# Performance work log

Measured on AMD Instinct MI355X. Metric: run time of the kernel, lower is better.

The kernel has to match this reference:

```python
import jax, jax.numpy as jnp
import numpy as np

NUM_HEADS = 32  # head_dim = input_dim // num_heads = 32 == C (forced by matmul contraction)


def setup_inputs() -> dict:
    key = jax.random.key(0)
    ks = jax.random.split(key, 8)
    B, C, D3, H1 = 16, 32, 1, 32
    input_dim = 1024  # == C**2, forced by the final view(B, C, H1, W1)
    s = 0.02
    x1 = jax.random.normal(ks[0], (B, C, D3, H1, input_dim), jnp.float32)
    x2 = jax.random.normal(ks[1], (B, C, D3, H1, input_dim), jnp.float32)
    Wq = jax.random.normal(ks[2], (input_dim, input_dim), jnp.float32) * s
    bq = jax.random.normal(ks[3], (input_dim,), jnp.float32) * s
    Wk = jax.random.normal(ks[4], (input_dim, input_dim), jnp.float32) * s
    bk = jax.random.normal(ks[5], (input_dim,), jnp.float32) * s
    Wv = jax.random.normal(ks[6], (input_dim, input_dim), jnp.float32) * s
    bv = jax.random.normal(ks[7], (input_dim,), jnp.float32) * s
    return {"x1": x1, "x2": x2, "Wq": Wq, "bq": bq, "Wk": Wk, "bk": bk, "Wv": Wv, "bv": bv}


def reference(x1, x2, Wq, bq, Wk, bk, Wv, bv):
    B, C, _, H1, W1 = x1.shape  # W1 == input_dim (Linear acts on last dim)
    nh = NUM_HEADS
    hd = W1 // nh
    # Linear projections on the last axis (torch Linear: x @ W.T + b)
    q = (x1 @ Wq.T + bq).reshape(B, C, nh, hd, -1).transpose(0, 2, 4, 3, 1)  # (B, nh, L1, hd, C)
    k = (x2 @ Wk.T + bk).reshape(B, C, nh, hd, -1)                            # (B, C, nh, hd, L2)
    v = (x2 @ Wv.T + bv).reshape(B, C, nh, hd, -1)                            # (B, C, nh, hd, L2)
    # Broadcasted batched matmul: contracts q's trailing C axis with k's hd axis (C == hd).
    energy = jnp.matmul(q, k)                      # (B, C, L1, hd, L2)
    attention = jax.nn.softmax(energy, axis=-1)    # softmax over L2
    # Contracts v's L2 axis with attention's hd axis (L2 == hd).
    out = jnp.matmul(v, attention)                 # (B, C, L1, hd, L2)
    out = out.transpose(0, 2, 4, 3, 1).reshape(B, C, H1, W1)
    return out
```

## Files before the change

### kernel.cpp

```cpp
#include <hip/hip_runtime.h>
#include <cstdint>

typedef __bf16 bf16x8 __attribute__((ext_vector_type(8)));
typedef float f32x4 __attribute__((ext_vector_type(4)));
typedef unsigned short us8 __attribute__((ext_vector_type(8)));

__device__ __forceinline__ unsigned short f2bf(float f) {
  union { float f; uint32_t u; } c; c.f = f;
  uint32_t u = c.u + 0x7FFFu + ((c.u >> 16) & 1u);
  return (unsigned short)(u >> 16);
}

__global__ __launch_bounds__(256) void cvt5(
    const float* __restrict__ x1, const float* __restrict__ x2,
    const float* __restrict__ Wq, const float* __restrict__ Wk, const float* __restrict__ Wv,
    unsigned short* __restrict__ xb1, unsigned short* __restrict__ xb2,
    unsigned short* __restrict__ wb) {
  int z = blockIdx.y;
  const float* src; unsigned short* dst; int n4;
  if (z == 0)      { src = x1; dst = xb1;            n4 = 16777216 / 4; }
  else if (z == 1) { src = x2; dst = xb2;            n4 = 16777216 / 4; }
  else if (z == 2) { src = Wq; dst = wb;             n4 = 1048576 / 4; }
  else if (z == 3) { src = Wk; dst = wb + 1048576;   n4 = 1048576 / 4; }
  else             { src = Wv; dst = wb + 2*1048576; n4 = 1048576 / 4; }
  for (int i = blockIdx.x * 256 + threadIdx.x; i < n4; i += gridDim.x * 256) {
    float4 v = ((const float4*)src)[i];
    ushort4 o;
    o.x = f2bf(v.x); o.y = f2bf(v.y); o.z = f2bf(v.z); o.w = f2bf(v.w);
    ((ushort4*)dst)[i] = o;
  }
}

__global__ __launch_bounds__(256) void gemm_qkv(
    const unsigned short* __restrict__ xb1, const unsigned short* __restrict__ xb2,
    const unsigned short* __restrict__ wb,
    const float* __restrict__ bq, const float* __restrict__ bk, const float* __restrict__ bv,
    unsigned short* __restrict__ qkv) {
  __shared__ __attribute__((aligned(16))) unsigned short lA[128 * 32];
  __shared__ __attribute__((aligned(16))) unsigned short lB[128 * 32];
  const int id = blockIdx.x;
  const int xcd = id & 7;
  const int j = id >> 3;
  const int nb = j & 7;
  const int g = j >> 3;
  const int z = g >> 4;
  const int mb = (g & 15) * 8 + xcd;
  const unsigned short* A = (z == 0) ? xb1 : xb2;
  const unsigned short* W = wb + z * 1048576;
  const float* bias = (z == 0) ? bq : (z == 1 ? bk : bv);
  unsigned short* C = qkv + z * 16777216;
  const int n0 = nb * 128;
  const int m0 = mb * 128;
  const int lane = threadIdx.x & 63;
  const int wv = threadIdx.x >> 6;
  const int wm = wv >> 1, wn = wv & 1;
  const int mr = lane & 15, quad = lane >> 4;

  f32x4 acc[4][4];
#pragma unroll
  for (int i = 0; i < 4; ++i)
#pragma unroll
    for (int jj = 0; jj < 4; ++jj) acc[i][jj] = (f32x4){0.f, 0.f, 0.f, 0.f};

  for (int k0 = 0; k0 < 1024; k0 += 32) {
#pragma unroll
    for (int c4 = 0; c4 < 4; ++c4) {
      int c = wv * 4 + c4;
      int isB = c >> 3;
      int cc = c & 7;
      int row = cc * 16 + (lane >> 2);
      const unsigned short* src = isB ? (W + (n0 + row) * 1024 + k0)
                                      : (A + (m0 + row) * 1024 + k0);
      const char* gp = (const char*)src + (lane & 3) * 16;
      char* ldst = (char*)(isB ? lB : lA) + cc * 1024;
      __builtin_amdgcn_global_load_lds((const __attribute__((address_space(1))) void*)gp,
                                       (__attribute__((address_space(3))) void*)ldst,
                                       16, 0, 0);
    }
    __syncthreads();
    bf16x8 af[4], bfr[4];
#pragma unroll
    for (int i = 0; i < 4; ++i)
      af[i] = *(const bf16x8*)(lA + (wm * 64 + i * 16 + mr) * 32 + quad * 8);
#pragma unroll
    for (int jj = 0; jj < 4; ++jj)
      bfr[jj] = *(const bf16x8*)(lB + (wn * 64 + jj * 16 + mr) * 32 + quad * 8);
#pragma unroll
    for (int i = 0; i < 4; ++i)
#pragma unroll
      for (int jj = 0; jj < 4; ++jj)
        acc[i][jj] = __builtin_amdgcn_mfma_f32_16x16x32_bf16(af[i], bfr[jj], acc[i][jj], 0, 0, 0);
    __syncthreads();
  }
#pragma unroll
  for (int jj = 0; jj < 4; ++jj) {
    int col = n0 + wn * 64 + jj * 16 + mr;
    float bb = bias[col];
#pragma unroll
    for (int i = 0; i < 4; ++i) {
      int rbase = m0 + wm * 64 + i * 16 + quad * 4;
#pragma unroll
      for (int r = 0; r < 4; ++r)
        C[(rbase + r) * 1024 + col] = f2bf(acc[i][jj][r] + bb);
    }
  }
}

__global__ __launch_bounds__(256) void attn(const unsigned short* __restrict__ qkv,
                                            float* __restrict__ obuf) {
  const unsigned short* qbuf = qkv;
  const unsigned short* kbuf = qkv + 16777216;
  const unsigned short* vbuf = qkv + 2 * 16777216;
  __shared__ __attribute__((aligned(16))) unsigned short qs[8192];
  __shared__ __attribute__((aligned(16))) unsigned short ks[4][1024];
  __shared__ __attribute__((aligned(16))) unsigned short vs[4][1024];
  __shared__ __attribute__((aligned(16))) unsigned short ats[4][1024];
  const int y0 = blockIdx.x * 8;
  const int x = blockIdx.y;
  const int b = blockIdx.z;
  const int lane = threadIdx.x & 63;
  const int wv = threadIdx.x >> 6;
  const int mr = lane & 15, quad = lane >> 4;

#pragma unroll
  for (int it = 0; it < 4; ++it) {
    int c = threadIdx.x + 256 * it;
    int t = c >> 5, m = c & 31;
    const uint4* src = (const uint4*)(qbuf + ((b * 1024 + t * 32 + x) * 1024 + m * 32 + y0));
    ((uint4*)qs)[c] = *src;
  }
  __syncthreads();

  for (int s = 0; s < 2; ++s) {
    int y = y0 + wv * 2 + s;
    int dy = wv * 2 + s;
    const unsigned short* krow = kbuf + ((b * 32 + x) * 32 + y) * 1024;
    const unsigned short* vrow = vbuf + ((b * 32 + x) * 32 + y) * 1024;
    ((uint4*)ks[wv])[lane] = ((const uint4*)krow)[lane];
    ((uint4*)ks[wv])[64 + lane] = ((const uint4*)krow)[64 + lane];
    ((uint4*)vs[wv])[lane] = ((const uint4*)vrow)[lane];
    ((uint4*)vs[wv])[64 + lane] = ((const uint4*)vrow)[64 + lane];

    bf16x8 qa[2], kb[2];
#pragma unroll
    for (int mt = 0; mt < 2; ++mt) {
      us8 tmp;
#pragma unroll
      for (int jj = 0; jj < 8; ++jj)
        tmp[jj] = qs[((quad * 8 + jj) * 32 + mt * 16 + mr) * 8 + dy];
      qa[mt] = __builtin_bit_cast(bf16x8, tmp);
    }
#pragma unroll
    for (int lt = 0; lt < 2; ++lt) {
      us8 tmp;
#pragma unroll
      for (int jj = 0; jj < 8; ++jj)
        tmp[jj] = ks[wv][(quad * 8 + jj) * 32 + lt * 16 + mr];
      kb[lt] = __builtin_bit_cast(bf16x8, tmp);
    }
    f32x4 e[2][2];
#pragma unroll
    for (int mt = 0; mt < 2; ++mt)
#pragma unroll
      for (int lt = 0; lt < 2; ++lt) {
        f32x4 zz = (f32x4){0.f, 0.f, 0.f, 0.f};
        e[mt][lt] = __builtin_amdgcn_mfma_f32_16x16x32_bf16(qa[mt], kb[lt], zz, 0, 0, 0);
      }

#pragma unroll
    for (int mt = 0; mt < 2; ++mt)
#pragma unroll
      for (int r = 0; r < 4; ++r) {
        float v0 = e[mt][0][r], v1 = e[mt][1][r];
        float mx = fmaxf(v0, v1);
#pragma unroll
        for (int off = 1; off < 16; off <<= 1) mx = fmaxf(mx, __shfl_xor(mx, off));
        float p0 = __expf(v0 - mx), p1 = __expf(v1 - mx);
        float sm = p0 + p1;
#pragma unroll
        for (int off = 1; off < 16; off <<= 1) sm += __shfl_xor(sm, off);
        float inv = 1.0f / sm;
        p0 *= inv; p1 *= inv;
        int trow = mt * 16 + quad * 4 + r;
        ats[wv][trow * 32 + mr] = f2bf(p0);
        ats[wv][trow * 32 + 16 + mr] = f2bf(p1);
      }

    bf16x8 va[2], pb[2];
#pragma unroll
    for (int i = 0; i < 2; ++i)
      va[i] = *(const bf16x8*)(&vs[wv][(i * 16 + mr) * 32 + quad * 8]);
#pragma unroll
    for (int lt = 0; lt < 2; ++lt) {
      us8 tmp;
#pragma unroll
      for (int jj = 0; jj < 8; ++jj)
        tmp[jj] = ats[wv][(quad * 8 + jj) * 32 + lt * 16 + mr];
      pb[lt] = __builtin_bit_cast(bf16x8, tmp);
    }
    f32x4 o[2][2];
#pragma unroll
    for (int i = 0; i < 2; ++i)
#pragma unroll
      for (int lt = 0; lt < 2; ++lt) {
        f32x4 zz = (f32x4){0.f, 0.f, 0.f, 0.f};
        o[i][lt] = __builtin_amdgcn_mfma_f32_16x16x32_bf16(va[i], pb[lt], zz, 0, 0, 0);
      }

    float* orow = obuf + ((b * 32 + x) * 32 + y) * 1024;
#pragma unroll
    for (int i = 0; i < 2; ++i)
#pragma unroll
      for (int lt = 0; lt < 2; ++lt)
#pragma unroll
        for (int r = 0; r < 4; ++r)
          orow[(i * 16 + quad * 4 + r) * 32 + lt * 16 + mr] = o[i][lt][r];
  }
}

__global__ __launch_bounds__(256) void transpose2(const float* __restrict__ obuf,
                                                  float* __restrict__ out) {
  __shared__ float t[32][33];
  const int m = blockIdx.x, y = blockIdx.y, b = blockIdx.z;
  int l = threadIdx.x & 31;
  int g = threadIdx.x >> 5;
  for (int xx = g; xx < 32; xx += 8)
    t[xx][l] = obuf[((b * 32 + xx) * 32 + y) * 1024 + m * 32 + l];
  __syncthreads();
  int xi = threadIdx.x & 31;
  for (int ll = g; ll < 32; ll += 8)
    out[((b * 32 + y) * 32 + ll) * 1024 + m * 32 + xi] = t[xi][ll];
}

extern "C" void kernel_launch(void* const* d_in, const int* in_sizes, int n_in,
                              void* d_out, int out_size, void* d_ws, size_t ws_size,
                              hipStream_t stream) {
  const float* x1 = (const float*)d_in[0];
  const float* x2 = (const float*)d_in[1];
  const float* Wq = (const float*)d_in[2];
  const float* bq = (const float*)d_in[3];
  const float* Wk = (const float*)d_in[4];
  const float* bk = (const float*)d_in[5];
  const float* Wv = (const float*)d_in[6];
  const float* bv = (const float*)d_in[7];
  float* out = (float*)d_out;

  char* ws = (char*)d_ws;
  unsigned short* xb1 = (unsigned short*)ws;
  unsigned short* xb2 = xb1 + 16777216;
  unsigned short* wb = xb2 + 16777216;
  unsigned short* qkv = wb + 3 * 1048576;
  float* obuf = (float*)ws;

  cvt5<<<dim3(2048, 5), 256, 0, stream>>>(x1, x2, Wq, Wk, Wv, xb1, xb2, wb);
  gemm_qkv<<<dim3(3072), 256, 0, stream>>>(xb1, xb2, wb, bq, bk, bv, qkv);
  attn<<<dim3(4, 32, 16), 256, 0, stream>>>(qkv, obuf);
  transpose2<<<dim3(32, 32, 16), 256, 0, stream>>>(obuf, out);
}
```

Baseline: 366.2 us.

## Load GEMM A fragments directly from global; batch transpose tiles per block

The QKV GEMM stops staging the activation tile A in LDS. Each wave now reads its A fragments straight from global memory into registers, and only the weight tile goes through LDS via global_load_lds. The transpose kernel now handles 8 column tiles per block, alternating between two shared buffers, which cuts the grid by 8x. The aim is less LDS traffic and fewer block launches, at the cost of uncoalesced 16-byte global loads for A and longer per-block serial work in the transpose.

```diff
diff --git a/kernel.cpp b/kernel.cpp
--- a/kernel.cpp
+++ b/kernel.cpp
@@ -36,7 +36,6 @@
     const unsigned short* __restrict__ wb,
     const float* __restrict__ bq, const float* __restrict__ bk, const float* __restrict__ bv,
     unsigned short* __restrict__ qkv) {
-  __shared__ __attribute__((aligned(16))) unsigned short lA[128 * 32];
   __shared__ __attribute__((aligned(16))) unsigned short lB[128 * 32];
   const int id = blockIdx.x;
   const int xcd = id & 7;
@@ -56,6 +55,8 @@
   const int wm = wv >> 1, wn = wv & 1;
   const int mr = lane & 15, quad = lane >> 4;
 
+  const unsigned short* Abase = A + (size_t)(m0 + wm * 64 + mr) * 1024 + quad * 8;
+
   f32x4 acc[4][4];
 #pragma unroll
   for (int i = 0; i < 4; ++i)
@@ -64,24 +65,22 @@
 
   for (int k0 = 0; k0 < 1024; k0 += 32) {
 #pragma unroll
-    for (int c4 = 0; c4 < 4; ++c4) {
-      int c = wv * 4 + c4;
-      int isB = c >> 3;
-      int cc = c & 7;
+    for (int c2 = 0; c2 < 2; ++c2) {
+      int cc = wv * 2 + c2;
       int row = cc * 16 + (lane >> 2);
-      const unsigned short* src = isB ? (W + (n0 + row) * 1024 + k0)
-                                      : (A + (m0 + row) * 1024 + k0);
+      const unsigned short* src = W + (n0 + row) * 1024 + k0;
       const char* gp = (const char*)src + (lane & 3) * 16;
-      char* ldst = (char*)(isB ? lB : lA) + cc * 1024;
+      char* ldst = (char*)lB + cc * 1024;
       __builtin_amdgcn_global_load_lds((const __attribute__((address_space(1))) void*)gp,
                                        (__attribute__((address_space(3))) void*)ldst,
                                        16, 0, 0);
     }
+    bf16x8 af[4];
+#pragma unroll
+    for (int i = 0; i < 4; ++i)
+      af[i] = *(const bf16x8*)(Abase + (size_t)i * 16 * 1024 + k0);
     __syncthreads();
-    bf16x8 af[4], bfr[4];
-#pragma unroll
-    for (int i = 0; i < 4; ++i)
-      af[i] = *(const bf16x8*)(lA + (wm * 64 + i * 16 + mr) * 32 + quad * 8);
+    bf16x8 bfr[4];
 #pragma unroll
     for (int jj = 0; jj < 4; ++jj)
       bfr[jj] = *(const bf16x8*)(lB + (wn * 64 + jj * 16 + mr) * 32 + quad * 8);
@@ -220,16 +219,20 @@
 
 __global__ __launch_bounds__(256) void transpose2(const float* __restrict__ obuf,
                                                   float* __restrict__ out) {
-  __shared__ float t[32][33];
-  const int m = blockIdx.x, y = blockIdx.y, b = blockIdx.z;
+  __shared__ float t[2][32][33];
+  const int y = blockIdx.y, b = blockIdx.z;
   int l = threadIdx.x & 31;
   int g = threadIdx.x >> 5;
-  for (int xx = g; xx < 32; xx += 8)
-    t[xx][l] = obuf[((b * 32 + xx) * 32 + y) * 1024 + m * 32 + l];
-  __syncthreads();
-  int xi = threadIdx.x & 31;
-  for (int ll = g; ll < 32; ll += 8)
-    out[((b * 32 + y) * 32 + ll) * 1024 + m * 32 + xi] = t[xi][ll];
+#pragma unroll
+  for (int mi = 0; mi < 8; ++mi) {
+    int m = blockIdx.x * 8 + mi;
+    int buf = mi & 1;
+    for (int xx = g; xx < 32; xx += 8)
+      t[buf][xx][l] = obuf[((b * 32 + xx) * 32 + y) * 1024 + m * 32 + l];
+    __syncthreads();
+    for (int ll = g; ll < 32; ll += 8)
+      out[((b * 32 + y) * 32 + ll) * 1024 + m * 32 + l] = t[buf][l][ll];
+  }
 }
 
 extern "C" void kernel_launch(void* const* d_in, const int* in_sizes, int n_in,
@@ -255,5 +258,5 @@
   cvt5<<<dim3(2048, 5), 256, 0, stream>>>(x1, x2, Wq, Wk, Wv, xb1, xb2, wb);
   gemm_qkv<<<dim3(3072), 256, 0, stream>>>(xb1, xb2, wb, bq, bk, bv, qkv);
   attn<<<dim3(4, 32, 16), 256, 0, stream>>>(qkv, obuf);
-  transpose2<<<dim3(32, 32, 16), 256, 0, stream>>>(obuf, out);
-}
+  transpose2<<<dim3(4, 32, 16), 256, 0, stream>>>(obuf, out);
+}
```

Result: slower. 458.2 us (+25.1%).
